# Kernel optimization log

Measured on AMD Instinct MI355X. Metric: run time of the kernel, lower is better.

The kernel has to match this reference:

```python
import jax, jax.numpy as jnp
import numpy as np

TAU = 0.1  # temperature from init

def setup_inputs() -> dict:
    key = jax.random.key(0)
    k1, k2 = jax.random.split(key)
    B, D, C = 8192, 128, 100
    z = jax.random.normal(k1, (B, D), dtype=jnp.float32)
    labels = jax.random.randint(k2, (B,), 0, C)
    return {"z": z, "labels": labels}

def reference(z, labels):
    # z: (B, D), labels: (B,)
    B = z.shape[0]
    sim = (z @ z.T) / TAU                              # (B, B)
    eye = jnp.eye(B, dtype=bool)
    sim_masked = jnp.where(eye, -jnp.inf, sim)         # self excluded
    # denominator: logsumexp over all non-self logits (diag is -inf -> contributes 0)
    lse = jax.nn.logsumexp(sim_masked, axis=1)         # (B,)
    pos_mask = (labels[:, None] == labels[None, :]) & ~eye
    n_pos = pos_mask.sum(axis=1)                       # (B,)
    pos_sum = jnp.where(pos_mask, sim, 0.0).sum(axis=1)
    # loss_i = -(mean over positives of (sim[i,j] - lse[i])) = lse[i] - pos_sum/n_pos
    loss_i = lse - pos_sum / jnp.maximum(n_pos, 1).astype(sim.dtype)
    valid = n_pos > 0                                  # anchors with >=1 positive
    n_valid = jnp.maximum(valid.sum(), 1).astype(sim.dtype)
    return jnp.where(valid, loss_i, 0.0).sum() / n_valid
```

## Files before the change

kernel.cpp:

```cpp
#include <hip/hip_runtime.h>
#include <hip/hip_bf16.h>

#define WB 8192
#define WD 128
#define WC 100
#define NSPLIT 16
#define JSPL (WB/NSPLIT)
#define NTT (JSPL/16)
#define NPH (NTT/4)
#define PITCH 272

typedef __attribute__((ext_vector_type(8))) short short8v;
typedef __attribute__((ext_vector_type(4))) float float4v;

#define SQS 3.798282f
#define LN2F 0.69314718055994531f

#define EXP2(x) __builtin_amdgcn_exp2f(x)
#define LOG2(x) __builtin_amdgcn_logf(x)

#define WS_ZBF   0u
#define WS_CNTP  2097152u
#define WS_ACC   2101248u
#define WS_LAB   2101264u
#define WS_PM    2109456u
#define WS_PL    2633744u
#define WS_PP    3158032u

__device__ __forceinline__ unsigned short f2bf(float x){
  unsigned u = __float_as_uint(x);
  u += 0x7fffu + ((u>>16)&1u);
  return (unsigned short)(u>>16);
}

__global__ __launch_bounds__(256) void k_prep(const float* __restrict__ z,
                                              const int* __restrict__ labels,
                                              unsigned short* __restrict__ zbf,
                                              unsigned* __restrict__ labu8,
                                              int* __restrict__ cntpart,
                                              float* accf, int* accn, int* ticket){
  const int bid = blockIdx.x, t = threadIdx.x;
  if (bid < 512){
    int idx = bid*256 + t;
    const float4* zi = (const float4*)z;
    float4 a = zi[idx*2], b = zi[idx*2+1];
    uint4 o;
    o.x = (unsigned)f2bf(a.x*SQS) | ((unsigned)f2bf(a.y*SQS)<<16);
    o.y = (unsigned)f2bf(a.z*SQS) | ((unsigned)f2bf(a.w*SQS)<<16);
    o.z = (unsigned)f2bf(b.x*SQS) | ((unsigned)f2bf(b.y*SQS)<<16);
    o.w = (unsigned)f2bf(b.z*SQS) | ((unsigned)f2bf(b.w*SQS)<<16);
    ((uint4*)zbf)[idx] = o;
    return;
  }
  __shared__ int hist[128];
  const int cb = bid - 512;
  if (t < 128) hist[t] = 0;
  if (bid == 512 && t == 0){ accf[0] = 0.f; accn[0] = 0; ticket[0] = 0; }
  __syncthreads();
  {
    int i = cb*1024 + t*4;
    int4 l4 = *(const int4*)(labels + i);
    labu8[cb*256 + t] = (unsigned)l4.x | ((unsigned)l4.y<<8)
                      | ((unsigned)l4.z<<16) | ((unsigned)l4.w<<24);
    atomicAdd(&hist[l4.x], 1); atomicAdd(&hist[l4.y], 1);
    atomicAdd(&hist[l4.z], 1); atomicAdd(&hist[l4.w], 1);
  }
  __syncthreads();
  if (t < 128) cntpart[cb*128 + t] = hist[t];
}

__global__ __launch_bounds__(256) void k_lse(const unsigned short* __restrict__ zbf,
                                             const int* __restrict__ labels,
                                             const unsigned* __restrict__ labu8,
                                             float* __restrict__ partM,
                                             float* __restrict__ partL,
                                             float* __restrict__ partPS){
  __shared__ __align__(16) unsigned char atile[2][64*PITCH];
  __shared__ unsigned ldslab[JSPL/4];
  const int t = threadIdx.x, wv = t>>6, lane = t&63;
  const int bid = blockIdx.x;
  const int xcd = bid & 7, chunk = bid >> 3;
  const int split = (xcd<<1) | (chunk & 1);
  const int ablk  = ((chunk>>1)<<2) | wv;
  const int awave = ablk*64;
  const int j0 = split*JSPL;
  const int lg = lane>>4, ln = lane&15;
  const bool DIAG = ((awave >> 9) == split);

  if (t < JSPL/4) ldslab[t] = labu8[(j0>>2) + t];

  short8v bf[4][4];
  int labA[4];
  #pragma unroll
  for (int ss = 0; ss < 4; ss++){
    const unsigned short* zr = zbf + (size_t)(awave + ss*16 + ln)*WD;
    #pragma unroll
    for (int kk = 0; kk < 4; kk++)
      bf[ss][kk] = *(const short8v*)(zr + kk*32 + lg*8);
    labA[ss] = labels[awave + ss*16 + ln];
  }

  float m[4], l[4], ps[4];
  #pragma unroll
  for (int ss = 0; ss < 4; ss++){ m[ss] = -INFINITY; l[ss] = 0.f; ps[ss] = 0.f; }

  const int srow0 = t>>4, sck = t&15;
  const unsigned short* sb = zbf + (size_t)(j0 + srow0)*WD + sck*8;
  const unsigned swbase = srow0*PITCH + sck*16;

  {
    uint4 s0 = *(const uint4*)(sb + (size_t)( 0)*WD);
    uint4 s1 = *(const uint4*)(sb + (size_t)(16)*WD);
    uint4 s2 = *(const uint4*)(sb + (size_t)(32)*WD);
    uint4 s3 = *(const uint4*)(sb + (size_t)(48)*WD);
    *(uint4*)&atile[0][swbase +  0*PITCH] = s0;
    *(uint4*)&atile[0][swbase + 16*PITCH] = s1;
    *(uint4*)&atile[0][swbase + 32*PITCH] = s2;
    *(uint4*)&atile[0][swbase + 48*PITCH] = s3;
  }
  __syncthreads();

  for (int ph = 0; ph < NPH; ph++){
    const int cur = ph & 1;
    uint4 nx0, nx1, nx2, nx3;
    const bool have = (ph+1 < NPH);
    if (have){
      const unsigned short* nb = sb + (size_t)((ph+1)*64)*WD;
      nx0 = *(const uint4*)(nb + (size_t)( 0)*WD);
      nx1 = *(const uint4*)(nb + (size_t)(16)*WD);
      nx2 = *(const uint4*)(nb + (size_t)(32)*WD);
      nx3 = *(const uint4*)(nb + (size_t)(48)*WD);
    }
    #pragma unroll
    for (int s = 0; s < 4; s++){
      const int tt = ph*4 + s;
      const int jb = j0 + tt*16;
      const unsigned lw = ldslab[tt*4 + lg];
      const int b0 = (int)(lw&255u),       b1 = (int)((lw>>8)&255u);
      const int b2 = (int)((lw>>16)&255u), b3 = (int)(lw>>24);
      const int rl = s*16 + ln;
      const unsigned rbase = rl*PITCH + lg*16;
      short8v af0 = *(const short8v*)&atile[cur][rbase +   0];
      short8v af1 = *(const short8v*)&atile[cur][rbase +  64];
      short8v af2 = *(const short8v*)&atile[cur][rbase + 128];
      short8v af3 = *(const short8v*)&atile[cur][rbase + 192];
      #pragma unroll
      for (int ss = 0; ss < 4; ss++){
        float4v acc = {0.f,0.f,0.f,0.f};
        acc = __builtin_amdgcn_mfma_f32_16x16x32_bf16(af0, bf[ss][0], acc, 0,0,0);
        acc = __builtin_amdgcn_mfma_f32_16x16x32_bf16(af1, bf[ss][1], acc, 0,0,0);
        acc = __builtin_amdgcn_mfma_f32_16x16x32_bf16(af2, bf[ss][2], acc, 0,0,0);
        acc = __builtin_amdgcn_mfma_f32_16x16x32_bf16(af3, bf[ss][3], acc, 0,0,0);
        float v0 = acc[0], v1 = acc[1], v2 = acc[2], v3 = acc[3];
        ps[ss] += ((b0==labA[ss]) ? v0 : 0.f) + ((b1==labA[ss]) ? v1 : 0.f)
                + ((b2==labA[ss]) ? v2 : 0.f) + ((b3==labA[ss]) ? v3 : 0.f);
        if (DIAG && jb == awave + ss*16){
          const int r0 = lg*4;
          if (r0+0 == ln){ ps[ss] -= v0; v0 = -INFINITY; }
          if (r0+1 == ln){ ps[ss] -= v1; v1 = -INFINITY; }
          if (r0+2 == ln){ ps[ss] -= v2; v2 = -INFINITY; }
          if (r0+3 == ln){ ps[ss] -= v3; v3 = -INFINITY; }
        }
        float tmax = fmaxf(fmaxf(v0,v1), fmaxf(v2,v3));
        float mn = fmaxf(m[ss], tmax);
        l[ss] = l[ss]*EXP2(m[ss]-mn)
              + ((EXP2(v0-mn) + EXP2(v1-mn)) + (EXP2(v2-mn) + EXP2(v3-mn)));
        m[ss] = mn;
      }
    }
    if (have){
      *(uint4*)&atile[cur^1][swbase +  0*PITCH] = nx0;
      *(uint4*)&atile[cur^1][swbase + 16*PITCH] = nx1;
      *(uint4*)&atile[cur^1][swbase + 32*PITCH] = nx2;
      *(uint4*)&atile[cur^1][swbase + 48*PITCH] = nx3;
    }
    __syncthreads();
  }

  #pragma unroll
  for (int ss = 0; ss < 4; ss++){
    float mm = m[ss], ll = l[ss], pp = ps[ss];
    #pragma unroll
    for (int off = 16; off < 64; off <<= 1){
      float mo = __shfl_xor(mm, off);
      float lo = __shfl_xor(ll, off);
      float M = fmaxf(mm, mo);
      ll = ll*EXP2(mm-M) + lo*EXP2(mo-M);
      mm = M;
      pp += __shfl_xor(pp, off);
    }
    if (lane < 16){
      size_t o = (size_t)split*WB + awave + ss*16 + lane;
      partM[o] = mm; partL[o] = ll; partPS[o] = pp;
    }
  }
}

__global__ __launch_bounds__(256) void k_final(const int* __restrict__ labels,
                                               const int* __restrict__ cntpart,
                                               const float* __restrict__ partM,
                                               const float* __restrict__ partL,
                                               const float* __restrict__ partPS,
                                               float* accf, int* accn, int* ticket,
                                               float* __restrict__ out){
  const int t = threadIdx.x;
  const int a = blockIdx.x*256 + t;
  float mm = -INFINITY;
  #pragma unroll 8
  for (int sp = 0; sp < NSPLIT; sp++)
    mm = fmaxf(mm, partM[(size_t)sp*WB + a]);
  float ll = 0.f, pp = 0.f;
  #pragma unroll 8
  for (int sp = 0; sp < NSPLIT; sp++){
    ll = fmaf(partL[(size_t)sp*WB + a], EXP2(partM[(size_t)sp*WB + a] - mm), ll);
    pp += partPS[(size_t)sp*WB + a];
  }
  float lse2 = mm + LOG2(ll);
  int lab = labels[a];
  int c = 0;
  #pragma unroll
  for (int b = 0; b < 8; b++) c += cntpart[b*128 + lab];
  int np = c - 1;
  float loss = 0.f, val = 0.f;
  if (np > 0){ loss = LN2F*(lse2 - pp/(float)np); val = 1.f; }
  #pragma unroll
  for (int off = 32; off > 0; off >>= 1){
    loss += __shfl_down(loss, off);
    val  += __shfl_down(val,  off);
  }
  __shared__ float sl[4], sv[4];
  int wv = t>>6, lane = t&63;
  if (lane == 0){ sl[wv] = loss; sv[wv] = val; }
  __syncthreads();
  if (t == 0){
    atomicAdd(accf, sl[0]+sl[1]+sl[2]+sl[3]);
    atomicAdd(accn, (int)(sv[0]+sv[1]+sv[2]+sv[3] + 0.5f));
    __threadfence();
    int tk = atomicAdd(ticket, 1);
    if (tk == 31){
      float f = atomicAdd(accf, 0.f);
      int   n = atomicAdd(accn, 0);
      out[0] = f / (float)max(n, 1);
    }
  }
}

extern "C" void kernel_launch(void* const* d_in, const int* in_sizes, int n_in,
                              void* d_out, int out_size, void* d_ws, size_t ws_size,
                              hipStream_t stream){
  const float* z = (const float*)d_in[0];
  const int* labels = (const int*)d_in[1];
  char* ws = (char*)d_ws;
  unsigned short* zbf = (unsigned short*)(ws + WS_ZBF);
  int*      cntp   = (int*)(ws + WS_CNTP);
  float*    accf   = (float*)(ws + WS_ACC);
  int*      accn   = (int*)(ws + WS_ACC + 4);
  int*      ticket = (int*)(ws + WS_ACC + 8);
  unsigned* labu8  = (unsigned*)(ws + WS_LAB);
  float*    partM  = (float*)(ws + WS_PM);
  float*    partL  = (float*)(ws + WS_PL);
  float*    partPS = (float*)(ws + WS_PP);
  float* out = (float*)d_out;

  hipLaunchKernelGGL(k_prep,  dim3(520), dim3(256), 0, stream,
                     z, labels, zbf, labu8, cntp, accf, accn, ticket);
  hipLaunchKernelGGL(k_lse,   dim3(512), dim3(256), 0, stream,
                     zbf, labels, labu8, partM, partL, partPS);
  hipLaunchKernelGGL(k_final, dim3(32),  dim3(256), 0, stream,
                     labels, cntp, partM, partL, partPS, accf, accn, ticket, out);
}
```

Measured before the change: 50.51 us.

## Split online softmax into separate row-max and exp-sum passes

Replaces the single online-logsumexp pass with two passes. The first recomputes the bf16 MFMA similarity tiles and takes each row's max through an order-preserving integer atomicMax. The second recomputes the tiles and sums exp2 against that fixed max, which drops the per-tile rescale exponentials and the max/merge bookkeeping. In exchange the whole GEMM runs twice and there is an extra kernel launch, so the approach only pays off if the exponential work was the bottleneck rather than the MFMA work.

```diff
diff --git a/kernel.cpp b/kernel.cpp
--- a/kernel.cpp
+++ b/kernel.cpp
@@ -23,14 +23,21 @@
 #define WS_CNTP  2097152u
 #define WS_ACC   2101248u
 #define WS_LAB   2101264u
-#define WS_PM    2109456u
-#define WS_PL    2633744u
-#define WS_PP    3158032u
+#define WS_RMAX  2109456u
+#define WS_PL    2142224u
+#define WS_PP    2666512u
 
 __device__ __forceinline__ unsigned short f2bf(float x){
   unsigned u = __float_as_uint(x);
   u += 0x7fffu + ((u>>16)&1u);
   return (unsigned short)(u>>16);
+}
+__device__ __forceinline__ unsigned fkey(float x){
+  unsigned u = __float_as_uint(x);
+  return (u>>31) ? ~u : (u | 0x80000000u);
+}
+__device__ __forceinline__ float fkeyinv(unsigned k){
+  return (k>>31) ? __uint_as_float(k & 0x7FFFFFFFu) : __uint_as_float(~k);
 }
 
 __global__ __launch_bounds__(256) void k_prep(const float* __restrict__ z,
@@ -38,6 +45,7 @@
                                               unsigned short* __restrict__ zbf,
                                               unsigned* __restrict__ labu8,
                                               int* __restrict__ cntpart,
+                                              unsigned* __restrict__ rmax,
                                               float* accf, int* accn, int* ticket){
   const int bid = blockIdx.x, t = threadIdx.x;
   if (bid < 512){
@@ -57,6 +65,7 @@
   if (t < 128) hist[t] = 0;
   if (bid == 512 && t == 0){ accf[0] = 0.f; accn[0] = 0; ticket[0] = 0; }
   __syncthreads();
+  for (int i = t; i < 1024; i += 256) rmax[cb*1024 + i] = 0u;
   {
     int i = cb*1024 + t*4;
     int4 l4 = *(const int4*)(labels + i);
@@ -69,10 +78,108 @@
   if (t < 128) cntpart[cb*128 + t] = hist[t];
 }
 
-__global__ __launch_bounds__(256) void k_lse(const unsigned short* __restrict__ zbf,
+__global__ __launch_bounds__(256) void k_max(const unsigned short* __restrict__ zbf,
+                                             unsigned* __restrict__ rmax){
+  __shared__ __align__(16) unsigned char atile[2][64*PITCH];
+  const int t = threadIdx.x, wv = t>>6, lane = t&63;
+  const int bid = blockIdx.x;
+  const int xcd = bid & 7, chunk = bid >> 3;
+  const int split = (xcd<<1) | (chunk & 1);
+  const int ablk  = ((chunk>>1)<<2) | wv;
+  const int awave = ablk*64;
+  const int j0 = split*JSPL;
+  const int lg = lane>>4, ln = lane&15;
+  const bool DIAG = ((awave >> 9) == split);
+
+  short8v bf[4][4];
+  #pragma unroll
+  for (int ss = 0; ss < 4; ss++){
+    const unsigned short* zr = zbf + (size_t)(awave + ss*16 + ln)*WD;
+    #pragma unroll
+    for (int kk = 0; kk < 4; kk++)
+      bf[ss][kk] = *(const short8v*)(zr + kk*32 + lg*8);
+  }
+  float m0[4], m1[4];
+  #pragma unroll
+  for (int ss = 0; ss < 4; ss++){ m0[ss] = -INFINITY; m1[ss] = -INFINITY; }
+
+  const int srow0 = t>>4, sck = t&15;
+  const unsigned short* sb = zbf + (size_t)(j0 + srow0)*WD + sck*8;
+  const unsigned swbase = srow0*PITCH + sck*16;
+  {
+    uint4 s0 = *(const uint4*)(sb + (size_t)( 0)*WD);
+    uint4 s1 = *(const uint4*)(sb + (size_t)(16)*WD);
+    uint4 s2 = *(const uint4*)(sb + (size_t)(32)*WD);
+    uint4 s3 = *(const uint4*)(sb + (size_t)(48)*WD);
+    *(uint4*)&atile[0][swbase +  0*PITCH] = s0;
+    *(uint4*)&atile[0][swbase + 16*PITCH] = s1;
+    *(uint4*)&atile[0][swbase + 32*PITCH] = s2;
+    *(uint4*)&atile[0][swbase + 48*PITCH] = s3;
+  }
+  __syncthreads();
+
+  for (int ph = 0; ph < NPH; ph++){
+    const int cur = ph & 1;
+    uint4 nx0, nx1, nx2, nx3;
+    const bool have = (ph+1 < NPH);
+    if (have){
+      const unsigned short* nb = sb + (size_t)((ph+1)*64)*WD;
+      nx0 = *(const uint4*)(nb + (size_t)( 0)*WD);
+      nx1 = *(const uint4*)(nb + (size_t)(16)*WD);
+      nx2 = *(const uint4*)(nb + (size_t)(32)*WD);
+      nx3 = *(const uint4*)(nb + (size_t)(48)*WD);
+    }
+    #pragma unroll
+    for (int s = 0; s < 4; s++){
+      const int tt = ph*4 + s;
+      const int jb = j0 + tt*16;
+      const int rl = s*16 + ln;
+      const unsigned rbase = rl*PITCH + lg*16;
+      short8v af0 = *(const short8v*)&atile[cur][rbase +   0];
+      short8v af1 = *(const short8v*)&atile[cur][rbase +  64];
+      short8v af2 = *(const short8v*)&atile[cur][rbase + 128];
+      short8v af3 = *(const short8v*)&atile[cur][rbase + 192];
+      #pragma unroll
+      for (int ss = 0; ss < 4; ss++){
+        float4v acc = {0.f,0.f,0.f,0.f};
+        acc = __builtin_amdgcn_mfma_f32_16x16x32_bf16(af0, bf[ss][0], acc, 0,0,0);
+        acc = __builtin_amdgcn_mfma_f32_16x16x32_bf16(af1, bf[ss][1], acc, 0,0,0);
+        acc = __builtin_amdgcn_mfma_f32_16x16x32_bf16(af2, bf[ss][2], acc, 0,0,0);
+        acc = __builtin_amdgcn_mfma_f32_16x16x32_bf16(af3, bf[ss][3], acc, 0,0,0);
+        float v0 = acc[0], v1 = acc[1], v2 = acc[2], v3 = acc[3];
+        if (DIAG && jb == awave + ss*16){
+          const int r0 = lg*4;
+          if (r0+0 == ln) v0 = -INFINITY;
+          if (r0+1 == ln) v1 = -INFINITY;
+          if (r0+2 == ln) v2 = -INFINITY;
+          if (r0+3 == ln) v3 = -INFINITY;
+        }
+        m0[ss] = fmaxf(m0[ss], fmaxf(v0,v1));
+        m1[ss] = fmaxf(m1[ss], fmaxf(v2,v3));
+      }
+    }
+    if (have){
+      *(uint4*)&atile[cur^1][swbase +  0*PITCH] = nx0;
+      *(uint4*)&atile[cur^1][swbase + 16*PITCH] = nx1;
+      *(uint4*)&atile[cur^1][swbase + 32*PITCH] = nx2;
+      *(uint4*)&atile[cur^1][swbase + 48*PITCH] = nx3;
+    }
+    __syncthreads();
+  }
+
+  #pragma unroll
+  for (int ss = 0; ss < 4; ss++){
+    float mm = fmaxf(m0[ss], m1[ss]);
+    mm = fmaxf(mm, __shfl_xor(mm, 16));
+    mm = fmaxf(mm, __shfl_xor(mm, 32));
+    if (lane < 16) atomicMax(&rmax[awave + ss*16 + lane], fkey(mm));
+  }
+}
+
+__global__ __launch_bounds__(256) void k_sum(const unsigned short* __restrict__ zbf,
                                              const int* __restrict__ labels,
                                              const unsigned* __restrict__ labu8,
-                                             float* __restrict__ partM,
+                                             const unsigned* __restrict__ rmax,
                                              float* __restrict__ partL,
                                              float* __restrict__ partPS){
   __shared__ __align__(16) unsigned char atile[2][64*PITCH];
@@ -91,6 +198,7 @@
 
   short8v bf[4][4];
   int labA[4];
+  float mf[4];
   #pragma unroll
   for (int ss = 0; ss < 4; ss++){
     const unsigned short* zr = zbf + (size_t)(awave + ss*16 + ln)*WD;
@@ -98,16 +206,15 @@
     for (int kk = 0; kk < 4; kk++)
       bf[ss][kk] = *(const short8v*)(zr + kk*32 + lg*8);
     labA[ss] = labels[awave + ss*16 + ln];
-  }
-
-  float m[4], l[4], ps[4];
-  #pragma unroll
-  for (int ss = 0; ss < 4; ss++){ m[ss] = -INFINITY; l[ss] = 0.f; ps[ss] = 0.f; }
+    mf[ss] = fkeyinv(rmax[awave + ss*16 + ln]);
+  }
+  float l0[4], l1[4], ps[4];
+  #pragma unroll
+  for (int ss = 0; ss < 4; ss++){ l0[ss] = 0.f; l1[ss] = 0.f; ps[ss] = 0.f; }
 
   const int srow0 = t>>4, sck = t&15;
   const unsigned short* sb = zbf + (size_t)(j0 + srow0)*WD + sck*8;
   const unsigned swbase = srow0*PITCH + sck*16;
-
   {
     uint4 s0 = *(const uint4*)(sb + (size_t)( 0)*WD);
     uint4 s1 = *(const uint4*)(sb + (size_t)(16)*WD);
@@ -161,11 +268,8 @@
           if (r0+2 == ln){ ps[ss] -= v2; v2 = -INFINITY; }
           if (r0+3 == ln){ ps[ss] -= v3; v3 = -INFINITY; }
         }
-        float tmax = fmaxf(fmaxf(v0,v1), fmaxf(v2,v3));
-        float mn = fmaxf(m[ss], tmax);
-        l[ss] = l[ss]*EXP2(m[ss]-mn)
-              + ((EXP2(v0-mn) + EXP2(v1-mn)) + (EXP2(v2-mn) + EXP2(v3-mn)));
-        m[ss] = mn;
+        l0[ss] += EXP2(v0-mf[ss]) + EXP2(v1-mf[ss]);
+        l1[ss] += EXP2(v2-mf[ss]) + EXP2(v3-mf[ss]);
       }
     }
     if (have){
@@ -179,43 +283,32 @@
 
   #pragma unroll
   for (int ss = 0; ss < 4; ss++){
-    float mm = m[ss], ll = l[ss], pp = ps[ss];
-    #pragma unroll
-    for (int off = 16; off < 64; off <<= 1){
-      float mo = __shfl_xor(mm, off);
-      float lo = __shfl_xor(ll, off);
-      float M = fmaxf(mm, mo);
-      ll = ll*EXP2(mm-M) + lo*EXP2(mo-M);
-      mm = M;
-      pp += __shfl_xor(pp, off);
-    }
+    float ll = l0[ss] + l1[ss], pp = ps[ss];
+    ll += __shfl_xor(ll, 16); pp += __shfl_xor(pp, 16);
+    ll += __shfl_xor(ll, 32); pp += __shfl_xor(pp, 32);
     if (lane < 16){
       size_t o = (size_t)split*WB + awave + ss*16 + lane;
-      partM[o] = mm; partL[o] = ll; partPS[o] = pp;
+      partL[o] = ll; partPS[o] = pp;
     }
   }
 }
 
 __global__ __launch_bounds__(256) void k_final(const int* __restrict__ labels,
                                                const int* __restrict__ cntpart,
-                                               const float* __restrict__ partM,
+                                               const unsigned* __restrict__ rmax,
                                                const float* __restrict__ partL,
                                                const float* __restrict__ partPS,
                                                float* accf, int* accn, int* ticket,
                                                float* __restrict__ out){
   const int t = threadIdx.x;
   const int a = blockIdx.x*256 + t;
-  float mm = -INFINITY;
-  #pragma unroll 8
-  for (int sp = 0; sp < NSPLIT; sp++)
-    mm = fmaxf(mm, partM[(size_t)sp*WB + a]);
   float ll = 0.f, pp = 0.f;
   #pragma unroll 8
   for (int sp = 0; sp < NSPLIT; sp++){
-    ll = fmaf(partL[(size_t)sp*WB + a], EXP2(partM[(size_t)sp*WB + a] - mm), ll);
+    ll += partL[(size_t)sp*WB + a];
     pp += partPS[(size_t)sp*WB + a];
   }
-  float lse2 = mm + LOG2(ll);
+  float lse2 = fkeyinv(rmax[a]) + LOG2(ll);
   int lab = labels[a];
   int c = 0;
   #pragma unroll
@@ -257,15 +350,16 @@
   int*      accn   = (int*)(ws + WS_ACC + 4);
   int*      ticket = (int*)(ws + WS_ACC + 8);
   unsigned* labu8  = (unsigned*)(ws + WS_LAB);
-  float*    partM  = (float*)(ws + WS_PM);
+  unsigned* rmax   = (unsigned*)(ws + WS_RMAX);
   float*    partL  = (float*)(ws + WS_PL);
   float*    partPS = (float*)(ws + WS_PP);
   float* out = (float*)d_out;
 
   hipLaunchKernelGGL(k_prep,  dim3(520), dim3(256), 0, stream,
-                     z, labels, zbf, labu8, cntp, accf, accn, ticket);
-  hipLaunchKernelGGL(k_lse,   dim3(512), dim3(256), 0, stream,
-                     zbf, labels, labu8, partM, partL, partPS);
+                     z, labels, zbf, labu8, cntp, rmax, accf, accn, ticket);
+  hipLaunchKernelGGL(k_max,   dim3(512), dim3(256), 0, stream, zbf, rmax);
+  hipLaunchKernelGGL(k_sum,   dim3(512), dim3(256), 0, stream,
+                     zbf, labels, labu8, rmax, partL, partPS);
   hipLaunchKernelGGL(k_final, dim3(32),  dim3(256), 0, stream,
-                     labels, cntp, partM, partL, partPS, accf, accn, ticket, out);
-}
+                     labels, cntp, rmax, partL, partPS, accf, accn, ticket, out);
+}
```

Result: slower. 62.02 us (+22.8%).
